# Performance work log

Hardware: AMD Instinct MI355X
Metric: run time of the kernel (lower is better)

The kernel has to match this reference:

```python
import jax, jax.numpy as jnp
import numpy as np

N_NODES = 100_000
N_CH = 16
DIM = 3
N_EDGES = 1_600_000
N_STEPS = 2
MAX_STEP_LEN = 1.0
EPS = jnp.float32(jnp.finfo(jnp.float32).eps)  # orig uses float64 eps; fp32-safe here


def setup_inputs() -> dict:
    key = jax.random.key(0)
    k1, k2, k3, k4, k5 = jax.random.split(key, 5)
    nodes = jax.random.normal(k1, (N_NODES, N_CH, DIM), dtype=jnp.float32)
    nodes = nodes / jnp.linalg.norm(nodes, axis=-1, keepdims=True)  # project to S^2
    senders = jax.random.randint(k2, (N_EDGES,), 0, N_NODES, dtype=jnp.int32)
    receivers = jax.random.randint(k3, (N_EDGES,), 0, N_NODES, dtype=jnp.int32)
    weights = jnp.ones((N_EDGES,), dtype=jnp.float32)
    # mimic truncated_normal(std=1)+1 inits (squared later => positive params)
    t_sqrt = 1.0 + 0.5 * jax.random.normal(k4, (N_CH,), dtype=jnp.float32)
    alpha_sqrt = 1.0 + 0.5 * jax.random.normal(k5, (N_CH,), dtype=jnp.float32)
    beta_sqrt = jnp.ones((N_CH,), dtype=jnp.float32)
    return dict(nodes=nodes, senders=senders, receivers=receivers, weights=weights,
                t_sqrt=t_sqrt, alpha_sqrt=alpha_sqrt, beta_sqrt=beta_sqrt)


def sphere_log(x, y):
    # log_x(y) on the unit sphere; x, y: (..., DIM)
    c = jnp.clip(jnp.sum(x * y, axis=-1, keepdims=True), -1.0 + 1e-7, 1.0 - 1e-7)
    theta = jnp.arccos(c)
    return (theta / jnp.sin(theta)) * (y - c * x)


def sphere_exp(x, v):
    # exp_x(v) on the unit sphere
    n = jnp.sqrt(jnp.sum(v * v, axis=-1, keepdims=True) + 1e-16)
    return jnp.cos(n) * x + (jnp.sin(n) / n) * v


def mfdg_laplace(nodes, senders, receivers, weights):
    # degree-normalized manifold graph Laplacian:
    #   L(x)_i = -(1/deg_i) * sum_{j in N(i)} w_ij log_{x_i}(x_j)
    logs = sphere_log(nodes[senders], nodes[receivers])         # (E, C, D)
    agg = jax.ops.segment_sum(weights[:, None, None] * logs, senders,
                              num_segments=N_NODES)             # (N, C, D)
    deg = jax.ops.segment_sum(weights, senders, num_segments=N_NODES)
    return -agg / (deg[:, None, None] + 1e-12)


def _flow(nodes, senders, receivers, weights, t_sqrt, alpha_sqrt, beta_sqrt):
    t = (t_sqrt ** 2) / N_STEPS   # (C,)
    a = alpha_sqrt ** 2           # (C,)
    b = beta_sqrt ** 2            # (C,)
    x = nodes
    for _ in range(N_STEPS):
        v = mfdg_laplace(x, senders, receivers, weights)        # (N, C, D)
        nrm = jnp.sqrt(jnp.sum(v * v, axis=-1) + EPS)           # (N, C)
        d = jax.nn.sigmoid(b * (nrm - a))                       # sigmoid gating
        scale = jnp.where(nrm * d <= MAX_STEP_LEN, d, MAX_STEP_LEN / nrm)
        v = -(v * scale[..., None]) * t[None, :, None]
        x = sphere_exp(x, v)
    return x


def reference(nodes, senders, receivers, weights, t_sqrt, alpha_sqrt, beta_sqrt):
    return _flow(nodes, senders, receivers, weights, t_sqrt, alpha_sqrt, beta_sqrt)
```

## Files before the change

kernel.cpp:

```cpp
#include <hip/hip_runtime.h>

#define N_NODES 100000
#define N_CH 16
#define DIM 3
#define N_EDGES 1600000
#define N_STEPS 2
#define EPS_D 1.1920928955078125e-7

#define PB 1024
#define NBLK ((N_NODES + PB - 1) / PB)
#define DBINS 64

__global__ void hist_kernel(const int4* __restrict__ senders4,
                            int* __restrict__ cnt) {
    int e = blockIdx.x * blockDim.x + threadIdx.x;
    if (e < N_EDGES / 4) {
        int4 s = senders4[e];
        atomicAdd(&cnt[s.x], 1);
        atomicAdd(&cnt[s.y], 1);
        atomicAdd(&cnt[s.z], 1);
        atomicAdd(&cnt[s.w], 1);
    }
}

__global__ void scan_partials(const int* __restrict__ cnt,
                              int* __restrict__ part) {
    __shared__ int sh[PB];
    int t = threadIdx.x;
    int g = blockIdx.x * PB + t;
    int v = (g < N_NODES) ? cnt[g] : 0;
    sh[t] = v;
    __syncthreads();
    for (int off = PB / 2; off > 0; off >>= 1) {
        if (t < off) sh[t] += sh[t + off];
        __syncthreads();
    }
    if (t == 0) part[blockIdx.x] = sh[0];
}

__global__ void scan_mid(int* __restrict__ part, int* __restrict__ rowptr) {
    __shared__ int sh[128];
    int t = threadIdx.x;
    int v = (t < NBLK) ? part[t] : 0;
    sh[t] = v;
    __syncthreads();
    for (int off = 1; off < 128; off <<= 1) {
        int u = (t >= off) ? sh[t - off] : 0;
        __syncthreads();
        sh[t] += u;
        __syncthreads();
    }
    if (t < NBLK) part[t] = sh[t] - v;
    if (t == NBLK - 1) rowptr[N_NODES] = sh[t];
}

__global__ void scan_apply(const int* __restrict__ cnt,
                           const int* __restrict__ part,
                           int* __restrict__ rowptr) {
    __shared__ int sh[PB];
    int t = threadIdx.x;
    int g = blockIdx.x * PB + t;
    int v = (g < N_NODES) ? cnt[g] : 0;
    sh[t] = v;
    __syncthreads();
    for (int off = 1; off < PB; off <<= 1) {
        int u = (t >= off) ? sh[t - off] : 0;
        __syncthreads();
        sh[t] += u;
        __syncthreads();
    }
    if (g < N_NODES) rowptr[g] = part[blockIdx.x] + sh[t] - v;
}

__global__ void dsort_hist(const int* __restrict__ cnt,
                           int* __restrict__ bins) {
    __shared__ int lb[DBINS];
    int t = threadIdx.x;
    if (t < DBINS) lb[t] = 0;
    __syncthreads();
    int g = blockIdx.x * blockDim.x + t;
    if (g < N_NODES) {
        int d = cnt[g]; if (d > DBINS - 1) d = DBINS - 1;
        atomicAdd(&lb[d], 1);
    }
    __syncthreads();
    if (t < DBINS && lb[t]) atomicAdd(&bins[t], lb[t]);
}

__global__ void dsort_scan(const int* __restrict__ bins,
                           int* __restrict__ binoff,
                           int* __restrict__ binfill) {
    int t = threadIdx.x;
    int v = bins[t];
    int s = v;
    for (int off = 1; off < DBINS; off <<= 1) {
        int u = __shfl_up(s, off, 64);
        if (t >= off) s += u;
    }
    binoff[t] = s - v;
    binfill[t] = 0;
}

__global__ void dsort_scatter(const int* __restrict__ cnt,
                              const int* __restrict__ binoff,
                              int* __restrict__ binfill,
                              int* __restrict__ perm) {
    __shared__ int lcnt[DBINS];
    __shared__ int lbase[DBINS];
    int t = threadIdx.x;
    if (t < DBINS) lcnt[t] = 0;
    __syncthreads();
    int g = blockIdx.x * blockDim.x + t;
    int d = 0, myoff = 0;
    if (g < N_NODES) {
        d = cnt[g]; if (d > DBINS - 1) d = DBINS - 1;
        myoff = atomicAdd(&lcnt[d], 1);
    }
    __syncthreads();
    if (t < DBINS && lcnt[t]) lbase[t] = atomicAdd(&binfill[t], lcnt[t]);
    __syncthreads();
    if (g < N_NODES) perm[binoff[d] + lbase[d] + myoff] = g;
}

__global__ void scatter_kernel(const int* __restrict__ senders,
                               const int* __restrict__ receivers,
                               const float* __restrict__ weights,
                               const int* __restrict__ rowptr,
                               int* __restrict__ cnt,
                               int2* __restrict__ edata) {
    int e = blockIdx.x * blockDim.x + threadIdx.x;
    if (e >= N_EDGES) return;
    int s = senders[e];
    int old = atomicAdd(&cnt[s], -1);
    edata[rowptr[s] + old - 1] = make_int2(receivers[e], __float_as_int(weights[e]));
}

__device__ __forceinline__ double fast_rsqrt(double x) {
    double y = (double)rsqrtf((float)x);
    y = y * fma(-0.5 * x, y * y, 1.5);
    return y;
}

__device__ __forceinline__ double theta_over_sin(double cd) {
    double acd = fabs(cd);
    bool mid = (acd <= 0.5);
    double z = mid ? (cd * cd) : (0.5 * (1.0 - acd));
    double A = 0.008390335809943149;
    A = fma(A, z, 0.009761609529194078);
    A = fma(A, z, 0.011551800896139706);
    A = fma(A, z, 0.013964843750);
    A = fma(A, z, 0.017352764423076924);
    A = fma(A, z, 0.022372159090909092);
    A = fma(A, z, 0.030381944444444444);
    A = fma(A, z, 0.044642857142857144);
    A = fma(A, z, 0.075);
    A = fma(A, z, 0.16666666666666666);
    A = fma(A, z, 1.0);
    double R = fast_rsqrt(1.0 - z);
    if (mid) return (1.5707963267948966 - cd * A) * R;
    double AR = A * R;
    if (cd > 0.0) return AR;
    double Rz = fast_rsqrt(z);
    return fma(1.5707963267948966 * Rz, R, -AR);
}

template <typename TI, typename TO>
__global__ void flow_kernel(const TI* __restrict__ x,
                            const int* __restrict__ rowptr,
                            const int2* __restrict__ edata,
                            const int* __restrict__ perm,
                            const float* __restrict__ t_sqrt,
                            const float* __restrict__ alpha_sqrt,
                            const float* __restrict__ beta_sqrt,
                            TO* __restrict__ xout) {
    int wave = threadIdx.x >> 6;
    int lane = threadIdx.x & 63;
    int q = lane >> 4;
    int c = lane & 15;
    int slot = (blockIdx.x * 4 + wave) * 4 + q;
    int i = perm ? perm[slot] : slot;

    int beg = rowptr[i];
    int end = rowptr[i + 1];

    const TI* xi = x + ((size_t)i * N_CH + c) * DIM;
    double ax = (double)xi[0], ay = (double)xi[1], az = (double)xi[2];

    double sx = 0.0, sy = 0.0, sz = 0.0, sw = 0.0;
    for (int k = beg; k < end; ++k) {
        int2 ed = edata[k];
        int r = ed.x;
        double w = (double)__int_as_float(ed.y);
        const TI* xr = x + ((size_t)r * N_CH + c) * DIM;
        double bx = (double)xr[0], by = (double)xr[1], bz = (double)xr[2];

        double cd = ax * bx + ay * by + az * bz;
        cd = fmin(fmax(cd, -1.0 + 1e-7), 1.0 - 1e-7);
        double f = w * theta_over_sin(cd);

        sx += f * (bx - cd * ax);
        sy += f * (by - cd * ay);
        sz += f * (bz - cd * az);
        sw += w;
    }

    double dg = sw + 1e-12;
    double inv = 1.0 / dg;
    double vx = -sx * inv, vy = -sy * inv, vz = -sz * inv;

    double t = (double)t_sqrt[c];     t = (t * t) / (double)N_STEPS;
    double a = (double)alpha_sqrt[c]; a = a * a;
    double b = (double)beta_sqrt[c];  b = b * b;

    double nrm = sqrt(vx * vx + vy * vy + vz * vz + EPS_D);
    double d = 1.0 / (1.0 + exp(-b * (nrm - a)));
    double scale = (nrm * d <= 1.0) ? d : (1.0 / nrm);
    double fs = -scale * t;
    vx *= fs; vy *= fs; vz *= fs;

    double n = sqrt(vx * vx + vy * vy + vz * vz + 1e-16);
    double cn = cos(n);
    double sf = sin(n) / n;

    TO* xo = xout + ((size_t)i * N_CH + c) * DIM;
    xo[0] = (TO)(cn * ax + sf * vx);
    xo[1] = (TO)(cn * ay + sf * vy);
    xo[2] = (TO)(cn * az + sf * vz);
}

__global__ void deg_kernel(const int* __restrict__ senders,
                           const float* __restrict__ weights,
                           float* __restrict__ deg) {
    int e = blockIdx.x * blockDim.x + threadIdx.x;
    if (e < N_EDGES) atomicAdd(&deg[senders[e]], weights[e]);
}

__global__ void edge_kernel(const float* __restrict__ x,
                            const int* __restrict__ senders,
                            const int* __restrict__ receivers,
                            const float* __restrict__ weights,
                            float* __restrict__ agg) {
    unsigned int tid = blockIdx.x * blockDim.x + threadIdx.x;
    if (tid >= (unsigned int)N_EDGES * N_CH) return;
    unsigned int e = tid >> 4;
    unsigned int c = tid & 15u;
    int s = senders[e];
    int r = receivers[e];
    float w = weights[e];
    const float* xs = x + ((size_t)s * N_CH + c) * DIM;
    const float* xr = x + ((size_t)r * N_CH + c) * DIM;
    float ax = xs[0], ay = xs[1], az = xs[2];
    float bx = xr[0], by = xr[1], bz = xr[2];
    float cd = ax * bx + ay * by + az * bz;
    cd = fminf(fmaxf(cd, -1.0f + 1e-7f), 1.0f - 1e-7f);
    float theta = acosf(cd);
    float sn = sqrtf(fmaxf(1.0f - cd * cd, 0.0f));
    float f = w * theta / sn;
    float* ag = agg + ((size_t)s * N_CH + c) * DIM;
    atomicAdd(&ag[0], f * (bx - cd * ax));
    atomicAdd(&ag[1], f * (by - cd * ay));
    atomicAdd(&ag[2], f * (bz - cd * az));
}

__global__ void node_kernel(const float* __restrict__ xin,
                            const float* __restrict__ agg,
                            const float* __restrict__ deg,
                            const float* __restrict__ t_sqrt,
                            const float* __restrict__ alpha_sqrt,
                            const float* __restrict__ beta_sqrt,
                            float* __restrict__ xout) {
    unsigned int tid = blockIdx.x * blockDim.x + threadIdx.x;
    if (tid >= (unsigned int)N_NODES * N_CH) return;
    unsigned int i = tid >> 4;
    unsigned int c = tid & 15u;
    float dg = deg[i] + 1e-12f;
    const float* ag = agg + (size_t)tid * DIM;
    float vx = -ag[0] / dg, vy = -ag[1] / dg, vz = -ag[2] / dg;
    float t = t_sqrt[c]; t = (t * t) * (1.0f / N_STEPS);
    float a = alpha_sqrt[c]; a = a * a;
    float b = beta_sqrt[c]; b = b * b;
    float nrm = sqrtf(vx * vx + vy * vy + vz * vz + 1.1920929e-7f);
    float d = 1.0f / (1.0f + __expf(-b * (nrm - a)));
    float scale = (nrm * d <= 1.0f) ? d : (1.0f / nrm);
    float fs = -scale * t;
    vx *= fs; vy *= fs; vz *= fs;
    const float* xi = xin + (size_t)tid * DIM;
    float axx = xi[0], ayy = xi[1], azz = xi[2];
    float n = sqrtf(vx * vx + vy * vy + vz * vz + 1e-16f);
    float cn = cosf(n);
    float sf = sinf(n) / n;
    float* xo = xout + (size_t)tid * DIM;
    xo[0] = cn * axx + sf * vx;
    xo[1] = cn * ayy + sf * vy;
    xo[2] = cn * azz + sf * vz;
}

extern "C" void kernel_launch(void* const* d_in, const int* in_sizes, int n_in,
                              void* d_out, int out_size, void* d_ws, size_t ws_size,
                              hipStream_t stream) {
    const float* nodes      = (const float*)d_in[0];
    const int*   senders    = (const int*)d_in[1];
    const int*   receivers  = (const int*)d_in[2];
    const float* weights    = (const float*)d_in[3];
    const float* t_sqrt     = (const float*)d_in[4];
    const float* alpha_sqrt = (const float*)d_in[5];
    const float* beta_sqrt  = (const float*)d_in[6];
    float* out = (float*)d_out;

    const size_t AL = 255;
    const size_t xtmp_b   = (size_t)N_NODES * N_CH * DIM * sizeof(double);
    const size_t rowptr_b = (((size_t)(N_NODES + 1) * sizeof(int)) + AL) & ~AL;
    const size_t cnt_b    = (((size_t)N_NODES * sizeof(int)) + AL) & ~AL;
    const size_t bins_b   = 1024;
    const size_t part_b   = 4096;
    const size_t perm_b   = (((size_t)N_NODES * sizeof(int)) + AL) & ~AL;
    const size_t edata_b  = (size_t)N_EDGES * sizeof(int2);
    const size_t need_sorted = xtmp_b + rowptr_b + cnt_b + bins_b + part_b + perm_b + edata_b;
    const size_t need_plain  = xtmp_b + rowptr_b + cnt_b + bins_b + part_b + edata_b;

    if (ws_size >= need_plain) {
        bool sorted = (ws_size >= need_sorted);
        char* p = (char*)d_ws;
        double* xtmp  = (double*)p;           p += xtmp_b;
        int*   rowptr = (int*)p;              p += rowptr_b;
        int*   cnt    = (int*)p;              p += cnt_b;
        int*   bins   = (int*)p;
        int*   binoff = bins + 64;
        int*   binfill= bins + 128;           p += bins_b;
        int*   part   = (int*)p;              p += part_b;
        int*   perm   = nullptr;
        if (sorted) { perm = (int*)p;         p += perm_b; }
        int2*  edata  = (int2*)p;

        hipMemsetAsync(cnt, 0, cnt_b + 256, stream);
        hist_kernel<<<(N_EDGES / 4 + 255) / 256, 256, 0, stream>>>(
            (const int4*)senders, cnt);
        scan_partials<<<NBLK, PB, 0, stream>>>(cnt, part);
        scan_mid<<<1, 128, 0, stream>>>(part, rowptr);
        scan_apply<<<NBLK, PB, 0, stream>>>(cnt, part, rowptr);
        if (sorted) {
            dsort_hist<<<NBLK, PB, 0, stream>>>(cnt, bins);
            dsort_scan<<<1, 64, 0, stream>>>(bins, binoff, binfill);
            dsort_scatter<<<NBLK, PB, 0, stream>>>(cnt, binoff, binfill, perm);
        }
        scatter_kernel<<<(N_EDGES + 255) / 256, 256, 0, stream>>>(
            senders, receivers, weights, rowptr, cnt, edata);

        int grid = N_NODES / 16;
        flow_kernel<float, double><<<grid, 256, 0, stream>>>(
            nodes, rowptr, edata, perm, t_sqrt, alpha_sqrt, beta_sqrt, xtmp);
        flow_kernel<double, float><<<grid, 256, 0, stream>>>(
            xtmp, rowptr, edata, perm, t_sqrt, alpha_sqrt, beta_sqrt, out);
    } else {
        float* agg = (float*)d_ws;
        float* deg = agg + (size_t)N_NODES * N_CH * DIM;
        hipMemsetAsync(deg, 0, N_NODES * sizeof(float), stream);
        deg_kernel<<<(N_EDGES + 255) / 256, 256, 0, stream>>>(senders, weights, deg);
        const float* xin = nodes;
        for (int step = 0; step < N_STEPS; ++step) {
            hipMemsetAsync(agg, 0, (size_t)N_NODES * N_CH * DIM * sizeof(float), stream);
            unsigned int n_ec = (unsigned int)N_EDGES * N_CH;
            edge_kernel<<<(n_ec + 255) / 256, 256, 0, stream>>>(xin, senders, receivers,
                                                                weights, agg);
            unsigned int n_nc = (unsigned int)N_NODES * N_CH;
            node_kernel<<<(n_nc + 255) / 256, 256, 0, stream>>>(xin, agg, deg, t_sqrt,
                                                                alpha_sqrt, beta_sqrt, out);
            xin = out;
        }
    }
}
```

Measured before the change: 375.5 us.

## Fuse degree-sort kernels into scan kernels and prefetch neighbor loads in flow loop

Merges the degree histogram, bin scan and permutation scatter into the three CSR prefix-scan kernels, removing three kernel launches and repeated reads of the count array. The flow kernel's edge loop is rewritten to software-pipeline neighbor loads two edges ahead, so gather latency overlaps with the trigonometric math. This raises register pressure in the double-precision flow kernel, which may lower occupancy.

```diff
diff --git a/kernel.cpp b/kernel.cpp
--- a/kernel.cpp
+++ b/kernel.cpp
@@ -23,10 +23,13 @@
     }
 }
 
-__global__ void scan_partials(const int* __restrict__ cnt,
-                              int* __restrict__ part) {
+__global__ void scan_partials_dhist(const int* __restrict__ cnt,
+                                    int* __restrict__ part,
+                                    int* __restrict__ bins) {
     __shared__ int sh[PB];
+    __shared__ int lb[DBINS];
     int t = threadIdx.x;
+    if (t < DBINS) lb[t] = 0;
     int g = blockIdx.x * PB + t;
     int v = (g < N_NODES) ? cnt[g] : 0;
     sh[t] = v;
@@ -36,9 +39,19 @@
         __syncthreads();
     }
     if (t == 0) part[blockIdx.x] = sh[0];
-}
-
-__global__ void scan_mid(int* __restrict__ part, int* __restrict__ rowptr) {
+    if (g < N_NODES) {
+        int d = (v > DBINS - 1) ? (DBINS - 1) : v;
+        atomicAdd(&lb[d], 1);
+    }
+    __syncthreads();
+    if (t < DBINS && lb[t]) atomicAdd(&bins[t], lb[t]);
+}
+
+__global__ void scan_mid_fused(int* __restrict__ part,
+                               int* __restrict__ rowptr,
+                               const int* __restrict__ bins,
+                               int* __restrict__ binoff,
+                               int* __restrict__ binfill) {
     __shared__ int sh[128];
     int t = threadIdx.x;
     int v = (t < NBLK) ? part[t] : 0;
@@ -52,74 +65,49 @@
     }
     if (t < NBLK) part[t] = sh[t] - v;
     if (t == NBLK - 1) rowptr[N_NODES] = sh[t];
-}
-
-__global__ void scan_apply(const int* __restrict__ cnt,
-                           const int* __restrict__ part,
-                           int* __restrict__ rowptr) {
+    if (t < DBINS) {
+        int bv = bins[t];
+        int s = bv;
+        for (int off = 1; off < DBINS; off <<= 1) {
+            int u = __shfl_up(s, off, 64);
+            if (t >= off) s += u;
+        }
+        binoff[t] = s - bv;
+        binfill[t] = 0;
+    }
+}
+
+__global__ void scan_apply_dscatter(const int* __restrict__ cnt,
+                                    const int* __restrict__ part,
+                                    int* __restrict__ rowptr,
+                                    const int* __restrict__ binoff,
+                                    int* __restrict__ binfill,
+                                    int* __restrict__ perm) {
     __shared__ int sh[PB];
-    int t = threadIdx.x;
-    int g = blockIdx.x * PB + t;
-    int v = (g < N_NODES) ? cnt[g] : 0;
-    sh[t] = v;
-    __syncthreads();
-    for (int off = 1; off < PB; off <<= 1) {
-        int u = (t >= off) ? sh[t - off] : 0;
-        __syncthreads();
-        sh[t] += u;
-        __syncthreads();
-    }
-    if (g < N_NODES) rowptr[g] = part[blockIdx.x] + sh[t] - v;
-}
-
-__global__ void dsort_hist(const int* __restrict__ cnt,
-                           int* __restrict__ bins) {
-    __shared__ int lb[DBINS];
-    int t = threadIdx.x;
-    if (t < DBINS) lb[t] = 0;
-    __syncthreads();
-    int g = blockIdx.x * blockDim.x + t;
-    if (g < N_NODES) {
-        int d = cnt[g]; if (d > DBINS - 1) d = DBINS - 1;
-        atomicAdd(&lb[d], 1);
-    }
-    __syncthreads();
-    if (t < DBINS && lb[t]) atomicAdd(&bins[t], lb[t]);
-}
-
-__global__ void dsort_scan(const int* __restrict__ bins,
-                           int* __restrict__ binoff,
-                           int* __restrict__ binfill) {
-    int t = threadIdx.x;
-    int v = bins[t];
-    int s = v;
-    for (int off = 1; off < DBINS; off <<= 1) {
-        int u = __shfl_up(s, off, 64);
-        if (t >= off) s += u;
-    }
-    binoff[t] = s - v;
-    binfill[t] = 0;
-}
-
-__global__ void dsort_scatter(const int* __restrict__ cnt,
-                              const int* __restrict__ binoff,
-                              int* __restrict__ binfill,
-                              int* __restrict__ perm) {
     __shared__ int lcnt[DBINS];
     __shared__ int lbase[DBINS];
     int t = threadIdx.x;
     if (t < DBINS) lcnt[t] = 0;
-    __syncthreads();
-    int g = blockIdx.x * blockDim.x + t;
+    int g = blockIdx.x * PB + t;
+    int v = (g < N_NODES) ? cnt[g] : 0;
+    sh[t] = v;
+    __syncthreads();
+    for (int off = 1; off < PB; off <<= 1) {
+        int u = (t >= off) ? sh[t - off] : 0;
+        __syncthreads();
+        sh[t] += u;
+        __syncthreads();
+    }
+    if (g < N_NODES) rowptr[g] = part[blockIdx.x] + sh[t] - v;
     int d = 0, myoff = 0;
     if (g < N_NODES) {
-        d = cnt[g]; if (d > DBINS - 1) d = DBINS - 1;
+        d = (v > DBINS - 1) ? (DBINS - 1) : v;
         myoff = atomicAdd(&lcnt[d], 1);
     }
     __syncthreads();
     if (t < DBINS && lcnt[t]) lbase[t] = atomicAdd(&binfill[t], lcnt[t]);
     __syncthreads();
-    if (g < N_NODES) perm[binoff[d] + lbase[d] + myoff] = g;
+    if (g < N_NODES && perm) perm[binoff[d] + lbase[d] + myoff] = g;
 }
 
 __global__ void scatter_kernel(const int* __restrict__ senders,
@@ -187,22 +175,38 @@
     double ax = (double)xi[0], ay = (double)xi[1], az = (double)xi[2];
 
     double sx = 0.0, sy = 0.0, sz = 0.0, sw = 0.0;
+
+    double b0x = 0, b0y = 0, b0z = 0, w0 = 0;
+    double b1x = 0, b1y = 0, b1z = 0, w1 = 0;
+
+#define LOADK(K, BX, BY, BZ, W)                                        \
+    {                                                                  \
+        int2 ed = edata[K];                                            \
+        W = (double)__int_as_float(ed.y);                              \
+        const TI* xr = x + ((size_t)ed.x * N_CH + c) * DIM;            \
+        BX = (double)xr[0]; BY = (double)xr[1]; BZ = (double)xr[2];    \
+    }
+
+    if (beg < end)      LOADK(beg,     b0x, b0y, b0z, w0);
+    if (beg + 1 < end)  LOADK(beg + 1, b1x, b1y, b1z, w1);
+
     for (int k = beg; k < end; ++k) {
-        int2 ed = edata[k];
-        int r = ed.x;
-        double w = (double)__int_as_float(ed.y);
-        const TI* xr = x + ((size_t)r * N_CH + c) * DIM;
-        double bx = (double)xr[0], by = (double)xr[1], bz = (double)xr[2];
-
-        double cd = ax * bx + ay * by + az * bz;
+        double b2x = 0, b2y = 0, b2z = 0, w2 = 0;
+        if (k + 2 < end) LOADK(k + 2, b2x, b2y, b2z, w2);
+
+        double cd = ax * b0x + ay * b0y + az * b0z;
         cd = fmin(fmax(cd, -1.0 + 1e-7), 1.0 - 1e-7);
-        double f = w * theta_over_sin(cd);
-
-        sx += f * (bx - cd * ax);
-        sy += f * (by - cd * ay);
-        sz += f * (bz - cd * az);
-        sw += w;
-    }
+        double f = w0 * theta_over_sin(cd);
+
+        sx += f * (b0x - cd * ax);
+        sy += f * (b0y - cd * ay);
+        sz += f * (b0z - cd * az);
+        sw += w0;
+
+        b0x = b1x; b0y = b1y; b0z = b1z; w0 = w1;
+        b1x = b2x; b1y = b2y; b1z = b2z; w1 = w2;
+    }
+#undef LOADK
 
     double dg = sw + 1e-12;
     double inv = 1.0 / dg;
@@ -335,14 +339,10 @@
         hipMemsetAsync(cnt, 0, cnt_b + 256, stream);
         hist_kernel<<<(N_EDGES / 4 + 255) / 256, 256, 0, stream>>>(
             (const int4*)senders, cnt);
-        scan_partials<<<NBLK, PB, 0, stream>>>(cnt, part);
-        scan_mid<<<1, 128, 0, stream>>>(part, rowptr);
-        scan_apply<<<NBLK, PB, 0, stream>>>(cnt, part, rowptr);
-        if (sorted) {
-            dsort_hist<<<NBLK, PB, 0, stream>>>(cnt, bins);
-            dsort_scan<<<1, 64, 0, stream>>>(bins, binoff, binfill);
-            dsort_scatter<<<NBLK, PB, 0, stream>>>(cnt, binoff, binfill, perm);
-        }
+        scan_partials_dhist<<<NBLK, PB, 0, stream>>>(cnt, part, bins);
+        scan_mid_fused<<<1, 128, 0, stream>>>(part, rowptr, bins, binoff, binfill);
+        scan_apply_dscatter<<<NBLK, PB, 0, stream>>>(cnt, part, rowptr,
+                                                     binoff, binfill, perm);
         scatter_kernel<<<(N_EDGES + 255) / 256, 256, 0, stream>>>(
             senders, receivers, weights, rowptr, cnt, edata);
 
```

Result: slower. 394.3 us (+5.0%).
